# Performance work log

Hardware: AMD Instinct MI355X
Metric: run time of the kernel (lower is better)

## Reference

```python
import jax, jax.numpy as jnp
import numpy as np

FACTORS = (32, 32, 32)  # prod = 32768 feature dim
BATCH = 2048


def setup_inputs() -> dict:
    key = jax.random.key(0)
    k0, k1, k2, k3 = jax.random.split(key, 4)
    N = int(np.prod(FACTORS))
    x = jax.random.normal(k0, (BATCH, N), dtype=jnp.float32)
    # scale weights ~1/sqrt(f) so outputs stay O(1) through 3 contractions
    s = 1.0 / np.sqrt(FACTORS[0])
    W1 = jax.random.normal(k1, (FACTORS[0], FACTORS[0]), dtype=jnp.float32) * s
    W2 = jax.random.normal(k2, (FACTORS[1], FACTORS[1]), dtype=jnp.float32) * s
    W3 = jax.random.normal(k3, (FACTORS[2], FACTORS[2]), dtype=jnp.float32) * s
    return {"x": x, "W1": W1, "W2": W2, "W3": W3}


def reference(x, W1, W2, W3):
    # Factorized (Kronecker) linear: y = x with each factor axis contracted
    # against its factor matrix (x.view(-1, f) @ W_f per factor, axes cycled).
    B = x.shape[0]
    f1, f2, f3 = FACTORS
    x = x.reshape(B, f1, f2, f3)
    x = jnp.einsum('bpqr,pi->biqr', x, W1)  # contract factor-1 axis
    x = jnp.einsum('biqr,qj->bijr', x, W2)  # contract factor-2 axis
    x = jnp.einsum('bijr,rk->bijk', x, W3)  # contract factor-3 axis
    return x.reshape(B, f1 * f2 * f3)
```

## Files before the change

kernel.cpp:

```cpp
#include <hip/hip_runtime.h>
#include <hip/hip_bf16.h>


typedef __attribute__((ext_vector_type(8))) short bf16x8;
typedef __attribute__((ext_vector_type(4))) float f32x4;

#define NROW 32768

__device__ __forceinline__ unsigned pk2(float a, float b) {
    union { __hip_bfloat162 h; unsigned u; } v;
    v.h = __float22bfloat162_rn(make_float2(a, b));
    return v.u;
}
__device__ __forceinline__ bf16x8 packfrag(float4 f0, float4 f1) {
    union { unsigned u[4]; bf16x8 b; } r;
    r.u[0] = pk2(f0.x, f0.y); r.u[1] = pk2(f0.z, f0.w);
    r.u[2] = pk2(f1.x, f1.y); r.u[3] = pk2(f1.z, f1.w);
    return r.b;
}

__device__ __forceinline__ int swz(int row, int col) {
    int s = ((row ^ (row >> 2) ^ (row >> 4)) & 3) << 3;
    return row * 32 + (col ^ s);
}

__device__ __forceinline__ bf16x8 wfrag(const float* __restrict__ W, int h, int c, int g) {
    union { unsigned u[4]; bf16x8 b; } r;
#pragma unroll
    for (int jj = 0; jj < 4; ++jj) {
        float a = W[(8 * g + 2 * jj    ) * 32 + 16 * h + c];
        float b = W[(8 * g + 2 * jj + 1) * 32 + 16 * h + c];
        r.u[jj] = pk2(a, b);
    }
    return r.b;
}

__device__ __forceinline__ bf16x8 ldsfrag(const unsigned short* buf, int row, int g) {
    int s = (row ^ (row >> 2) ^ (row >> 4)) & 3;
    union { uint4 u; bf16x8 b; } cv;
    cv.u = *(const uint4*)(buf + row * 32 + 8 * (g ^ s));
    return cv.b;
}

__global__ __launch_bounds__(1024, 8) void kron3_mfma(
    const float* __restrict__ x,  const float* __restrict__ W1,
    const float* __restrict__ W2, const float* __restrict__ W3,
    float* __restrict__ out)
{
    __shared__ unsigned short buf[NROW];
    const int t = threadIdx.x;
    const int w = t >> 6, c = t & 15, g = (t >> 4) & 3;
    const float* __restrict__ xrow = x + (size_t)blockIdx.x * NROW;
    float* __restrict__ orow = out + (size_t)blockIdx.x * NROW;
    const f32x4 vzero = {0.f, 0.f, 0.f, 0.f};

    bf16x8 fa[4];
#pragma unroll
    for (int mt = 0; mt < 4; ++mt) {
        const float* s = xrow + (64 * w + 16 * mt + c) * 32 + 8 * g;
        float4 f0 = ((const float4*)s)[0];
        float4 f1 = ((const float4*)s)[1];
        fa[mt] = packfrag(f0, f1);
    }
    bf16x8 wA[2] = { wfrag(W3, 0, c, g), wfrag(W3, 1, c, g) };

#pragma unroll
    for (int nt = 0; nt < 2; ++nt) {
        const int kp = 16 * nt + c;
#pragma unroll
        for (int mt = 0; mt < 4; ++mt) {
            f32x4 a = __builtin_amdgcn_mfma_f32_16x16x32_bf16(fa[mt], wA[nt], vzero, 0, 0, 0);
            const int p  = 2 * w + (mt >> 1);
            const int q0 = 16 * (mt & 1) + 4 * g;
            *(uint2*)(buf + swz(kp * 32 + p, q0)) =
                make_uint2(pk2(a[0], a[1]), pk2(a[2], a[3]));
        }
    }
    __syncthreads();

    bf16x8 fb[4];
#pragma unroll
    for (int mt = 0; mt < 4; ++mt)
        fb[mt] = ldsfrag(buf, 64 * w + 16 * mt + c, g);
    bf16x8 wB[2] = { wfrag(W2, 0, c, g), wfrag(W2, 1, c, g) };
    __syncthreads();

#pragma unroll
    for (int nt = 0; nt < 2; ++nt) {
        const int j = 16 * nt + c;
#pragma unroll
        for (int mt = 0; mt < 4; ++mt) {
            f32x4 a = __builtin_amdgcn_mfma_f32_16x16x32_bf16(fb[mt], wB[nt], vzero, 0, 0, 0);
            const int kq = 2 * w + (mt >> 1);
            const int p0 = 16 * (mt & 1) + 4 * g;
            *(uint2*)(buf + swz(j * 32 + kq, p0)) =
                make_uint2(pk2(a[0], a[1]), pk2(a[2], a[3]));
        }
    }
    __syncthreads();

    bf16x8 fc[4];
#pragma unroll
    for (int mt = 0; mt < 4; ++mt)
        fc[mt] = ldsfrag(buf, 64 * w + 16 * mt + c, g);
    bf16x8 wC[2] = { wfrag(W1, 0, c, g), wfrag(W1, 1, c, g) };

#pragma unroll
    for (int nt = 0; nt < 2; ++nt) {
        const int i = 16 * nt + c;
#pragma unroll
        for (int mt = 0; mt < 4; ++mt) {
            f32x4 a = __builtin_amdgcn_mfma_f32_16x16x32_bf16(fc[mt], wC[nt], vzero, 0, 0, 0);
            const int j  = 2 * w + (mt >> 1);
            const int k0 = 16 * (mt & 1) + 4 * g;
            __builtin_nontemporal_store(a,
                (f32x4*)(orow + i * 1024 + j * 32 + k0));
        }
    }
}

extern "C" void kernel_launch(void* const* d_in, const int* in_sizes, int n_in,
                              void* d_out, int out_size, void* d_ws, size_t ws_size,
                              hipStream_t stream) {
    const float* x  = (const float*)d_in[0];
    const float* W1 = (const float*)d_in[1];
    const float* W2 = (const float*)d_in[2];
    const float* W3 = (const float*)d_in[3];
    float* outp = (float*)d_out;

    const int batch = in_sizes[0] / NROW;
    kron3_mfma<<<dim3(batch), dim3(1024), 0, stream>>>(x, W1, W2, W3, outp);
}
```

Baseline: 121.2 us.

## Split each batch row across two blocks by output-k half

Each batch row is now handled by two 512-thread blocks, each computing half of the last-factor (W3) output columns. Each block uses 32 KB of shared memory instead of 64 KB, so more blocks can be resident and scheduled at finer grain. The cost is that every block reads the full input row, doubling input reads, although the second read may hit in cache. The nontemporal output stores are also replaced with plain float4 stores.

```diff
diff --git a/kernel.cpp b/kernel.cpp
--- a/kernel.cpp
+++ b/kernel.cpp
@@ -42,37 +42,31 @@
     return cv.b;
 }
 
-__global__ __launch_bounds__(1024, 8) void kron3_mfma(
+__global__ __launch_bounds__(512, 4) void kron3_half(
     const float* __restrict__ x,  const float* __restrict__ W1,
     const float* __restrict__ W2, const float* __restrict__ W3,
     float* __restrict__ out)
 {
-    __shared__ unsigned short buf[NROW];
+    __shared__ unsigned short buf[16384];
     const int t = threadIdx.x;
     const int w = t >> 6, c = t & 15, g = (t >> 4) & 3;
-    const float* __restrict__ xrow = x + (size_t)blockIdx.x * NROW;
-    float* __restrict__ orow = out + (size_t)blockIdx.x * NROW;
+    const int h = blockIdx.x & 1;
+    const float* __restrict__ xrow = x   + (size_t)(blockIdx.x >> 1) * NROW;
+    float* __restrict__       orow = out + (size_t)(blockIdx.x >> 1) * NROW;
     const f32x4 vzero = {0.f, 0.f, 0.f, 0.f};
 
-    bf16x8 fa[4];
+    {
+        const bf16x8 wA = wfrag(W3, h, c, g);
 #pragma unroll
-    for (int mt = 0; mt < 4; ++mt) {
-        const float* s = xrow + (64 * w + 16 * mt + c) * 32 + 8 * g;
-        float4 f0 = ((const float4*)s)[0];
-        float4 f1 = ((const float4*)s)[1];
-        fa[mt] = packfrag(f0, f1);
-    }
-    bf16x8 wA[2] = { wfrag(W3, 0, c, g), wfrag(W3, 1, c, g) };
-
-#pragma unroll
-    for (int nt = 0; nt < 2; ++nt) {
-        const int kp = 16 * nt + c;
-#pragma unroll
-        for (int mt = 0; mt < 4; ++mt) {
-            f32x4 a = __builtin_amdgcn_mfma_f32_16x16x32_bf16(fa[mt], wA[nt], vzero, 0, 0, 0);
-            const int p  = 2 * w + (mt >> 1);
+        for (int mt = 0; mt < 8; ++mt) {
+            const float* s = xrow + (128 * w + 16 * mt + c) * 32 + 8 * g;
+            float4 f0 = ((const float4*)s)[0];
+            float4 f1 = ((const float4*)s)[1];
+            f32x4 a = __builtin_amdgcn_mfma_f32_16x16x32_bf16(
+                packfrag(f0, f1), wA, vzero, 0, 0, 0);
+            const int p  = 4 * w + (mt >> 1);
             const int q0 = 16 * (mt & 1) + 4 * g;
-            *(uint2*)(buf + swz(kp * 32 + p, q0)) =
+            *(uint2*)(buf + swz(c * 32 + p, q0)) =
                 make_uint2(pk2(a[0], a[1]), pk2(a[2], a[3]));
         }
     }
@@ -82,19 +76,20 @@
 #pragma unroll
     for (int mt = 0; mt < 4; ++mt)
         fb[mt] = ldsfrag(buf, 64 * w + 16 * mt + c, g);
-    bf16x8 wB[2] = { wfrag(W2, 0, c, g), wfrag(W2, 1, c, g) };
     __syncthreads();
 
+    {
+        bf16x8 wB[2] = { wfrag(W2, 0, c, g), wfrag(W2, 1, c, g) };
 #pragma unroll
-    for (int nt = 0; nt < 2; ++nt) {
-        const int j = 16 * nt + c;
+        for (int jt = 0; jt < 2; ++jt) {
 #pragma unroll
-        for (int mt = 0; mt < 4; ++mt) {
-            f32x4 a = __builtin_amdgcn_mfma_f32_16x16x32_bf16(fb[mt], wB[nt], vzero, 0, 0, 0);
-            const int kq = 2 * w + (mt >> 1);
-            const int p0 = 16 * (mt & 1) + 4 * g;
-            *(uint2*)(buf + swz(j * 32 + kq, p0)) =
-                make_uint2(pk2(a[0], a[1]), pk2(a[2], a[3]));
+            for (int mt = 0; mt < 4; ++mt) {
+                f32x4 a = __builtin_amdgcn_mfma_f32_16x16x32_bf16(fb[mt], wB[jt], vzero, 0, 0, 0);
+                const int row = (16 * jt + c) * 16 + 2 * w + (mt >> 1);
+                const int p0  = 16 * (mt & 1) + 4 * g;
+                *(uint2*)(buf + swz(row, p0)) =
+                    make_uint2(pk2(a[0], a[1]), pk2(a[2], a[3]));
+            }
         }
     }
     __syncthreads();
@@ -103,18 +98,20 @@
 #pragma unroll
     for (int mt = 0; mt < 4; ++mt)
         fc[mt] = ldsfrag(buf, 64 * w + 16 * mt + c, g);
-    bf16x8 wC[2] = { wfrag(W1, 0, c, g), wfrag(W1, 1, c, g) };
 
+    {
+        bf16x8 wC[2] = { wfrag(W1, 0, c, g), wfrag(W1, 1, c, g) };
 #pragma unroll
-    for (int nt = 0; nt < 2; ++nt) {
-        const int i = 16 * nt + c;
+        for (int nt = 0; nt < 2; ++nt) {
+            const int i = 16 * nt + c;
 #pragma unroll
-        for (int mt = 0; mt < 4; ++mt) {
-            f32x4 a = __builtin_amdgcn_mfma_f32_16x16x32_bf16(fc[mt], wC[nt], vzero, 0, 0, 0);
-            const int j  = 2 * w + (mt >> 1);
-            const int k0 = 16 * (mt & 1) + 4 * g;
-            __builtin_nontemporal_store(a,
-                (f32x4*)(orow + i * 1024 + j * 32 + k0));
+            for (int mt = 0; mt < 4; ++mt) {
+                f32x4 a = __builtin_amdgcn_mfma_f32_16x16x32_bf16(fc[mt], wC[nt], vzero, 0, 0, 0);
+                const int j  = 4 * w + mt;
+                const int k0 = 16 * h + 4 * g;
+                *(float4*)(orow + i * 1024 + j * 32 + k0) =
+                    make_float4(a[0], a[1], a[2], a[3]);
+            }
         }
     }
 }
@@ -129,5 +126,5 @@
     float* outp = (float*)d_out;
 
     const int batch = in_sizes[0] / NROW;
-    kron3_mfma<<<dim3(batch), dim3(1024), 0, stream>>>(x, W1, W2, W3, outp);
+    kron3_half<<<dim3(batch * 2), dim3(512), 0, stream>>>(x, W1, W2, W3, outp);
 }
```

Result: slower. 156.7 us (+29.3%).
